# Optimization experiments

Hardware: AMD Instinct MI355X
Metric: run time of the kernel (lower is better)

The kernel has to match this reference:

```python
import jax, jax.numpy as jnp
import numpy as np

N_NODES = 50000
N_EDGES = 600000
N_GRAPHS = 256
BN_EPS = 1e-5
NEG_SLOPE = 0.2  # PyG GATv2 default leaky_relu slope


def segment_softmax(logits, seg, num_segments):
    # logits: [E, H], softmax over edges sharing the same destination node
    m = jax.ops.segment_max(logits, seg, num_segments=num_segments)
    e = jnp.exp(logits - m[seg])
    s = jax.ops.segment_sum(e, seg, num_segments=num_segments)
    return e / (s[seg] + 1e-16)


def gatv2_layer(h, edge_attr, src, dst, Wl, bl, Wr, br, We, att, bias, concat):
    # PyG GATv2Conv (share_weights=False, edge_dim set), eval mode (no dropout)
    heads, out_c = att.shape
    N = h.shape[0]
    xl = (h @ Wl + bl).reshape(N, heads, out_c)  # messages from source
    xr = (h @ Wr + br).reshape(N, heads, out_c)  # destination term
    em = (edge_attr @ We).reshape(-1, heads, out_c)
    z = jax.nn.leaky_relu(xl[src] + xr[dst] + em, NEG_SLOPE)  # [E,H,C]
    logits = jnp.einsum('ehc,hc->eh', z, att)
    alpha = segment_softmax(logits, dst, N)  # [E,H]
    out = jax.ops.segment_sum(xl[src] * alpha[:, :, None], dst, num_segments=N)
    out = out.reshape(N, heads * out_c) if concat else out.mean(axis=1)
    return out + bias


def batch_norm(h, gamma, beta):
    mu = h.mean(axis=0)
    var = h.var(axis=0)
    return gamma * (h - mu) * jax.lax.rsqrt(var + BN_EPS) + beta


def setup_inputs() -> dict:
    key = jax.random.key(0)
    ks = jax.random.split(key, 32)
    F, Fe, H, C = 64, 16, 4, 64
    HC = H * C

    def w(k, shape):
        return jax.random.normal(k, shape, dtype=jnp.float32) * 0.1

    inp = {
        'x': jax.random.normal(ks[0], (N_NODES, F), dtype=jnp.float32),
        'edge_attr': jax.random.normal(ks[1], (N_EDGES, Fe), dtype=jnp.float32),
        'edge_index': jax.random.randint(ks[2], (2, N_EDGES), 0, N_NODES, dtype=jnp.int32),
        'batch': jnp.sort(jax.random.randint(ks[3], (N_NODES,), 0, N_GRAPHS, dtype=jnp.int32)),
        # input projection
        'W_in': w(ks[4], (F, C)), 'b_in': jnp.zeros((C,), jnp.float32),
        'Wl0': w(ks[5], (C, HC)), 'bl0': jnp.zeros((HC,), jnp.float32),
        'Wr0': w(ks[6], (C, HC)), 'br0': jnp.zeros((HC,), jnp.float32),
        'We0': w(ks[7], (Fe, HC)),
        'att0': w(ks[8], (H, C)), 'bias0': jnp.zeros((HC,), jnp.float32),
        'g0': jnp.ones((HC,), jnp.float32), 'beta0': jnp.zeros((HC,), jnp.float32),
        'Wl1': w(ks[9], (HC, HC)), 'bl1': jnp.zeros((HC,), jnp.float32),
        'Wr1': w(ks[10], (HC, HC)), 'br1': jnp.zeros((HC,), jnp.float32),
        'We1': w(ks[11], (Fe, HC)),
        'att1': w(ks[12], (H, C)), 'bias1': jnp.zeros((C,), jnp.float32),
        'g1': jnp.ones((C,), jnp.float32), 'beta1': jnp.zeros((C,), jnp.float32),
        # MLP head 64 -> 32 -> 16 -> 1
        'Wm1': w(ks[13], (C, C // 2)), 'bm1': jnp.zeros((C // 2,), jnp.float32),
        'Wm2': w(ks[14], (C // 2, C // 4)), 'bm2': jnp.zeros((C // 4,), jnp.float32),
        'Wm3': w(ks[15], (C // 4, 1)), 'bm3': jnp.zeros((1,), jnp.float32),
    }
    return inp


def reference(x, edge_attr, W_in, b_in,
              Wl0, bl0, Wr0, br0, We0, att0, bias0, g0, beta0,
              Wl1, bl1, Wr1, br1, We1, att1, bias1, g1, beta1,
              Wm1, bm1, Wm2, bm2, Wm3, bm3,
              edge_index, batch):
    src, dst = edge_index[0], edge_index[1]
    h = jax.nn.relu(x @ W_in + b_in)
    h = gatv2_layer(h, edge_attr, src, dst, Wl0, bl0, Wr0, br0, We0, att0, bias0, True)
    h = batch_norm(h, g0, beta0)
    h = jax.nn.relu(h)  # dropout is identity in eval mode
    h = gatv2_layer(h, edge_attr, src, dst, Wl1, bl1, Wr1, br1, We1, att1, bias1, False)
    h = batch_norm(h, g1, beta1)
    # global mean pool over graphs
    cnt = jax.ops.segment_sum(jnp.ones((h.shape[0],), h.dtype), batch, num_segments=N_GRAPHS)
    pooled = jax.ops.segment_sum(h, batch, num_segments=N_GRAPHS) / jnp.maximum(cnt, 1.0)[:, None]
    z = jax.nn.relu(pooled @ Wm1 + bm1)
    z = jax.nn.relu(z @ Wm2 + bm2)
    return z @ Wm3 + bm3  # [N_GRAPHS, 1]
```

## Files before the change

### kernel.cpp

```cpp
#include <hip/hip_runtime.h>
#include <math.h>

constexpr int NN = 50000;
constexpr int NE = 600000;
constexpr int NG = 256;
constexpr int SB = (NN + 255) / 256;
constexpr float kBnEps = 1e-5f;
constexpr float kSlope = 0.2f;

typedef _Float16 f16x8 __attribute__((ext_vector_type(8)));
typedef float f32x16 __attribute__((ext_vector_type(16)));

__device__ __forceinline__ float rdlane(float v, int l) {
    return __builtin_bit_cast(float, __builtin_amdgcn_readlane(__builtin_bit_cast(int, v), l));
}

template <int CTRL>
__device__ __forceinline__ float dppadd(float v) {
    int t = __builtin_amdgcn_mov_dpp(__builtin_bit_cast(int, v), CTRL, 0xF, 0xF, true);
    return v + __builtin_bit_cast(float, t);
}
__device__ __forceinline__ float sum16(float v) {
    v = dppadd<0xB1>(v);
    v = dppadd<0x4E>(v);
    v = dppadd<0x141>(v);
    v = dppadd<0x140>(v);
    return v;
}

__device__ __forceinline__ float4 fma4(float a, float4 b, float4 c) {
    c.x = fmaf(a, b.x, c.x); c.y = fmaf(a, b.y, c.y);
    c.z = fmaf(a, b.z, c.z); c.w = fmaf(a, b.w, c.w);
    return c;
}

__global__ __launch_bounds__(256) void k_hist(const int* __restrict__ dst, int* __restrict__ cnt)
{
    int e = blockIdx.x * 256 + threadIdx.x;
    if (e < NE) atomicAdd(&cnt[dst[e]], 1);
}

__global__ __launch_bounds__(256) void k_scanA(const int* __restrict__ cnt,
                                               int* __restrict__ offs, int* __restrict__ bsum)
{
    __shared__ int s[256];
    int tid = threadIdx.x;
    int i = blockIdx.x * 256 + tid;
    int v = (i < NN) ? cnt[i] : 0;
    s[tid] = v;
    __syncthreads();
    #pragma unroll
    for (int d = 1; d < 256; d <<= 1) {
        int u = (tid >= d) ? s[tid - d] : 0;
        __syncthreads();
        s[tid] += u;
        __syncthreads();
    }
    if (i < NN) offs[i] = s[tid];
    if (tid == 255) bsum[blockIdx.x] = s[255];
}

__global__ __launch_bounds__(256) void k_scanC(const int* __restrict__ cnt,
                                               const int* __restrict__ bsum,
                                               int* __restrict__ offs, int* __restrict__ cur)
{
    __shared__ int sred[256];
    int t = threadIdx.x;
    int b = blockIdx.x;
    int v = (t < SB && t < b) ? bsum[t] : 0;
    sred[t] = v;
    __syncthreads();
    #pragma unroll
    for (int d = 128; d > 0; d >>= 1) {
        if (t < d) sred[t] += sred[t + d];
        __syncthreads();
    }
    int pre = sred[0];
    int i = b * 256 + t;
    if (i > NN) return;
    if (i == NN) { offs[NN] = NE; return; }
    int w = offs[i] - cnt[i] + pre;
    offs[i] = w;
    cur[i] = w;
}

__global__ __launch_bounds__(256) void k_scatter_light(const int* __restrict__ dst,
                                                       const int* __restrict__ src,
                                                       int* __restrict__ cur,
                                                       int2* __restrict__ se)
{
    int e = blockIdx.x * 256 + threadIdx.x;
    if (e < NE) {
        int p = atomicAdd(&cur[dst[e]], 1);
        se[p] = make_int2(src[e], e);
    }
}

__device__ __forceinline__ void prep_w_body(int T, const float* __restrict__ WL,
                                            const float* __restrict__ WR,
                                            _Float16* __restrict__ bhi,
                                            _Float16* __restrict__ blo)
{
    int g   = T & 1;
    int col = (T >> 1) & 511;
    int kt  = T >> 10;
    const float* W = (col < 256) ? WL : WR;
    int c = col & 255;
    f16x8 h8, l8;
    #pragma unroll
    for (int i = 0; i < 8; ++i) {
        float v = W[(size_t)(kt * 16 + g * 8 + i) * 256 + c];
        _Float16 hv = (_Float16)v;
        h8[i] = hv;
        l8[i] = (_Float16)(v - (float)hv);
    }
    *(f16x8*)(bhi + (size_t)T * 8) = h8;
    *(f16x8*)(blo + (size_t)T * 8) = l8;
}

__global__ __launch_bounds__(256) void k_prep_all(
    const float* __restrict__ Wl0, const float* __restrict__ Wr0,
    _Float16* __restrict__ bhi0, _Float16* __restrict__ blo0,
    const float* __restrict__ Wl1, const float* __restrict__ Wr1,
    _Float16* __restrict__ bhi1, _Float16* __restrict__ blo1)
{
    if (blockIdx.x < 16) {
        int T = blockIdx.x * 256 + threadIdx.x;
        prep_w_body(T, Wl0, Wr0, bhi0, blo0);
    } else {
        int T = (blockIdx.x - 16) * 256 + threadIdx.x;
        prep_w_body(T, Wl1, Wr1, bhi1, blo1);
    }
}

__global__ __launch_bounds__(512) void k_lin0_mfma(
    const float* __restrict__ x, const float* __restrict__ Win,
    const float* __restrict__ bin,
    const _Float16* __restrict__ Bhi, const _Float16* __restrict__ Blo,
    const float* __restrict__ bl, const float* __restrict__ br,
    float* __restrict__ outl, float* __restrict__ outr)
{
    __shared__ float h0s[64][68];
    __shared__ f16x8 Apack[2][4][128];
    int tid = threadIdx.x;
    int lane = tid & 63, wave = tid >> 6;
    int row0 = blockIdx.x * 64;

    {
        int rbase = row0 + wave * 8;
        float xreg[8];
        #pragma unroll
        for (int j = 0; j < 8; ++j) {
            int row = rbase + j; if (row >= NN) row = NN - 1;
            xreg[j] = x[(size_t)row * 64 + lane];
        }
        float b0 = bin[lane];
        float h0r[8];
        #pragma unroll
        for (int j = 0; j < 8; ++j) h0r[j] = b0;
        for (int k = 0; k < 64; ++k) {
            float w = Win[k * 64 + lane];
            #pragma unroll
            for (int j = 0; j < 8; ++j) h0r[j] = fmaf(rdlane(xreg[j], k), w, h0r[j]);
        }
        #pragma unroll
        for (int j = 0; j < 8; ++j)
            h0s[wave * 8 + j][lane] = fmaxf(h0r[j], 0.f);
    }
    __syncthreads();

    {
        int row = tid >> 3;
        int o = (tid & 7) * 8;
        f16x8 hi8, lo8;
        #pragma unroll
        for (int i = 0; i < 8; ++i) {
            float v = h0s[row][o + i];
            _Float16 hv = (_Float16)v;
            hi8[i] = hv;
            lo8[i] = (_Float16)(v - (float)hv);
        }
        int kt = o >> 4, g2 = (o >> 3) & 1;
        int slot = (g2 * 64 + row) ^ kt;
        Apack[0][kt][slot] = hi8;
        Apack[1][kt][slot] = lo8;
    }
    __syncthreads();

    int g = lane >> 5;
    int rowtile = wave >> 2;
    int colbase = (wave & 3) * 128 + (lane & 31);
    int aslot = g * 64 + rowtile * 32 + (lane & 31);
    f32x16 acc[4];
    #pragma unroll
    for (int nt = 0; nt < 4; ++nt)
        #pragma unroll
        for (int r = 0; r < 16; ++r) acc[nt][r] = 0.f;

    const f16x8* bh = (const f16x8*)Bhi;
    const f16x8* bo = (const f16x8*)Blo;
    size_t fbase = (size_t)colbase * 2 + g;

    #pragma unroll 1
    for (int kt = 0; kt < 4; ++kt) {
        f16x8 ahi = Apack[0][kt][aslot ^ kt];
        f16x8 alo = Apack[1][kt][aslot ^ kt];
        f16x8 wh[4], wl[4];
        #pragma unroll
        for (int nt = 0; nt < 4; ++nt) {
            size_t fi = fbase + (size_t)kt * 1024 + nt * 64;
            wh[nt] = bh[fi];
            wl[nt] = bo[fi];
        }
        #pragma unroll
        for (int nt = 0; nt < 4; ++nt)
            acc[nt] = __builtin_amdgcn_mfma_f32_32x32x16_f16(ahi, wh[nt], acc[nt], 0, 0, 0);
        #pragma unroll
        for (int nt = 0; nt < 4; ++nt)
            acc[nt] = __builtin_amdgcn_mfma_f32_32x32x16_f16(alo, wh[nt], acc[nt], 0, 0, 0);
        #pragma unroll
        for (int nt = 0; nt < 4; ++nt)
            acc[nt] = __builtin_amdgcn_mfma_f32_32x32x16_f16(ahi, wl[nt], acc[nt], 0, 0, 0);
    }

    #pragma unroll
    for (int nt = 0; nt < 4; ++nt) {
        int col = colbase + nt * 32;
        bool isR = col >= 256;
        int c = isR ? col - 256 : col;
        float bv = isR ? br[c] : bl[c];
        float* outp = isR ? outr : outl;
        #pragma unroll
        for (int r = 0; r < 16; ++r) {
            int rowoff = (r & 3) + 8 * (r >> 2) + 4 * g;
            int grow = row0 + rowtile * 32 + rowoff;
            if (grow < NN)
                outp[(size_t)grow * 256 + c] = acc[nt][r] + bv;
        }
    }
}

__global__ __launch_bounds__(256) void k_linear2_mfma(
    const float* __restrict__ h, const _Float16* __restrict__ Bhi,
    const _Float16* __restrict__ Blo, const float* __restrict__ bl,
    const float* __restrict__ br, const float* __restrict__ scale,
    const float* __restrict__ shift, float* __restrict__ outl,
    float* __restrict__ outr)
{
    __shared__ f16x8 Apack[2][16][64];
    int tid = threadIdx.x;
    int lane = tid & 63, wave = tid >> 6;
    int q = blockIdx.x & 3;
    int mslot = blockIdx.x >> 2;
    int g = lane >> 5;
    int colbase = q * 128 + wave * 32 + (lane & 31);
    size_t fbase = (size_t)colbase * 2 + g;

    const f16x8* bh = (const f16x8*)Bhi;
    const f16x8* bo = (const f16x8*)Blo;
    f16x8 BH[16], BL[16];
    #pragma unroll
    for (int kt = 0; kt < 16; ++kt) {
        BH[kt] = bh[fbase + (size_t)kt * 1024];
        BL[kt] = bo[fbase + (size_t)kt * 1024];
    }

    bool isR = colbase >= 256;
    int c = isR ? colbase - 256 : colbase;
    float bv = isR ? br[c] : bl[c];
    float* outp = isR ? outr : outl;

    constexpr int NT = (NN + 31) / 32;
    for (int t = mslot; t < NT; t += 128) {
        int row0 = t * 32;
        {
            int row  = tid >> 3;
            int koff = (tid & 7) * 32;
            int grow = row0 + row; if (grow >= NN) grow = NN - 1;
            const float* hp = h + (size_t)grow * 256 + koff;
            #pragma unroll
            for (int j2 = 0; j2 < 4; ++j2) {
                int o = koff + j2 * 8;
                float4 a  = *(const float4*)(hp + j2 * 8);
                float4 b  = *(const float4*)(hp + j2 * 8 + 4);
                float4 s0 = *(const float4*)(scale + o);
                float4 s1 = *(const float4*)(scale + o + 4);
                float4 f0 = *(const float4*)(shift + o);
                float4 f1 = *(const float4*)(shift + o + 4);
                float va[8] = {
                    fmaxf(fmaf(a.x, s0.x, f0.x), 0.f), fmaxf(fmaf(a.y, s0.y, f0.y), 0.f),
                    fmaxf(fmaf(a.z, s0.z, f0.z), 0.f), fmaxf(fmaf(a.w, s0.w, f0.w), 0.f),
                    fmaxf(fmaf(b.x, s1.x, f1.x), 0.f), fmaxf(fmaf(b.y, s1.y, f1.y), 0.f),
                    fmaxf(fmaf(b.z, s1.z, f1.z), 0.f), fmaxf(fmaf(b.w, s1.w, f1.w), 0.f)};
                f16x8 hi8, lo8;
                #pragma unroll
                for (int i = 0; i < 8; ++i) {
                    _Float16 hv = (_Float16)va[i];
                    hi8[i] = hv;
                    lo8[i] = (_Float16)(va[i] - (float)hv);
                }
                int kt = o >> 4, g2 = (o >> 3) & 1;
                int slot = (g2 * 32 + row) ^ (kt & 7);
                Apack[0][kt][slot] = hi8;
                Apack[1][kt][slot] = lo8;
            }
        }
        __syncthreads();

        f32x16 acc;
        #pragma unroll
        for (int r = 0; r < 16; ++r) acc[r] = 0.f;

        #pragma unroll
        for (int kt = 0; kt < 16; ++kt) {
            f16x8 ahi = Apack[0][kt][lane ^ (kt & 7)];
            f16x8 alo = Apack[1][kt][lane ^ (kt & 7)];
            acc = __builtin_amdgcn_mfma_f32_32x32x16_f16(ahi, BH[kt], acc, 0, 0, 0);
            acc = __builtin_amdgcn_mfma_f32_32x32x16_f16(alo, BH[kt], acc, 0, 0, 0);
            acc = __builtin_amdgcn_mfma_f32_32x32x16_f16(ahi, BL[kt], acc, 0, 0, 0);
        }
        __syncthreads();

        #pragma unroll
        for (int r = 0; r < 16; ++r) {
            int rowoff = (r & 3) + 8 * (r >> 2) + 4 * g;
            int grow = row0 + rowoff;
            if (grow < NN)
                outp[(size_t)grow * 256 + c] = acc[r] + bv;
        }
    }
}

template <bool CONCAT, int NPW>
__global__ __launch_bounds__(256) void k_attn(
    const float* __restrict__ xl, const float* __restrict__ xr,
    const int2* __restrict__ se, const float* __restrict__ ea,
    const float* __restrict__ We, const float* __restrict__ att,
    const int* __restrict__ offs, const float* __restrict__ bias,
    float* __restrict__ out)
{
    int tid = threadIdx.x;
    int lane = tid & 63, wave = tid >> 6;
    float4 wr[16];
    #pragma unroll
    for (int k = 0; k < 16; ++k) wr[k] = ((const float4*)(We + k * 256))[lane];
    float4 ar = ((const float4*)att)[lane];

    int g16 = lane >> 4;
    int k16 = lane & 15;
    int nodebase = (blockIdx.x * 4 + wave) * NPW;
    if (nodebase >= NN) return;

    for (int nn = 0; nn < NPW; ++nn) {
        int n = nodebase + nn;
        if (n >= NN) break;
        int beg = offs[n], end = offs[n + 1];
        float4 xr4 = ((const float4*)(xr + (size_t)n * 256))[lane];

        float m = -INFINITY, ssum = 0.f;
        float4 acc = make_float4(0.f, 0.f, 0.f, 0.f);

        float nea = 0.f;
        float4 nx0, nx1, nx2, nx3;

        auto loadbatch = [&](int i) {
            int idx = i + g16;
            if (idx > end - 1) idx = end - 1;
            int2 sv2 = se[idx];
            nea = ea[(size_t)sv2.y * 16 + k16];
            int sv = sv2.x;
            int s0 = __builtin_amdgcn_readlane(sv, 0);
            int s1 = __builtin_amdgcn_readlane(sv, 16);
            int s2 = __builtin_amdgcn_readlane(sv, 32);
            int s3 = __builtin_amdgcn_readlane(sv, 48);
            nx0 = ((const float4*)(xl + (size_t)s0 * 256))[lane];
            nx1 = ((const float4*)(xl + (size_t)s1 * 256))[lane];
            nx2 = ((const float4*)(xl + (size_t)s2 * 256))[lane];
            nx3 = ((const float4*)(xl + (size_t)s3 * 256))[lane];
        };

        if (beg < end) loadbatch(beg);

        for (int i = beg; i < end; i += 4) {
            float cea = nea;
            float4 x0 = nx0, x1 = nx1, x2 = nx2, x3 = nx3;
            if (i + 4 < end) loadbatch(i + 4);

            float p[4];
            #pragma unroll
            for (int g = 0; g < 4; ++g) {
                float4 xg = (g == 0) ? x0 : (g == 1) ? x1 : (g == 2) ? x2 : x3;
                float4 em = xr4;
                #pragma unroll
                for (int k = 0; k < 16; ++k) {
                    float a = rdlane(cea, g * 16 + k);
                    em.x = fmaf(a, wr[k].x, em.x);
                    em.y = fmaf(a, wr[k].y, em.y);
                    em.z = fmaf(a, wr[k].z, em.z);
                    em.w = fmaf(a, wr[k].w, em.w);
                }
                float z0 = xg.x + em.x;
                float z1 = xg.y + em.y;
                float z2 = xg.z + em.z;
                float z3 = xg.w + em.w;
                z0 = (z0 > 0.f) ? z0 : kSlope * z0;
                z1 = (z1 > 0.f) ? z1 : kSlope * z1;
                z2 = (z2 > 0.f) ? z2 : kSlope * z2;
                z3 = (z3 > 0.f) ? z3 : kSlope * z3;
                float pv = fmaf(z0, ar.x, fmaf(z1, ar.y, fmaf(z2, ar.z, z3 * ar.w)));
                pv = sum16(pv);
                p[g] = (i + g < end) ? pv : -INFINITY;
            }
            float pm = fmaxf(fmaxf(p[0], p[1]), fmaxf(p[2], p[3]));
            float mn = fmaxf(m, pm);
            float sc = __expf(m - mn);
            float w0 = __expf(p[0] - mn);
            float w1 = __expf(p[1] - mn);
            float w2 = __expf(p[2] - mn);
            float w3 = __expf(p[3] - mn);
            ssum = fmaf(ssum, sc, (w0 + w1) + (w2 + w3));
            acc.x = fmaf(acc.x, sc, fmaf(w0, x0.x, fmaf(w1, x1.x, fmaf(w2, x2.x, w3 * x3.x))));
            acc.y = fmaf(acc.y, sc, fmaf(w0, x0.y, fmaf(w1, x1.y, fmaf(w2, x2.y, w3 * x3.y))));
            acc.z = fmaf(acc.z, sc, fmaf(w0, x0.z, fmaf(w1, x1.z, fmaf(w2, x2.z, w3 * x3.z))));
            acc.w = fmaf(acc.w, sc, fmaf(w0, x0.w, fmaf(w1, x1.w, fmaf(w2, x2.w, w3 * x3.w))));
            m = mn;
        }

        float inv = 1.f / (ssum + 1e-16f);
        if (CONCAT) {
            float4 b4 = ((const float4*)bias)[lane];
            float4 o;
            o.x = fmaf(acc.x, inv, b4.x);
            o.y = fmaf(acc.y, inv, b4.y);
            o.z = fmaf(acc.z, inv, b4.z);
            o.w = fmaf(acc.w, inv, b4.w);
            ((float4*)(out + (size_t)n * 256))[lane] = o;
        } else {
            float v0 = acc.x * inv, v1 = acc.y * inv, v2 = acc.z * inv, v3 = acc.w * inv;
            v0 += __shfl_xor(v0, 16, 64); v0 += __shfl_xor(v0, 32, 64);
            v1 += __shfl_xor(v1, 16, 64); v1 += __shfl_xor(v1, 32, 64);
            v2 += __shfl_xor(v2, 16, 64); v2 += __shfl_xor(v2, 32, 64);
            v3 += __shfl_xor(v3, 16, 64); v3 += __shfl_xor(v3, 32, 64);
            if (lane < 16) {
                float4 b4 = ((const float4*)bias)[lane];
                float4 o;
                o.x = fmaf(0.25f, v0, b4.x);
                o.y = fmaf(0.25f, v1, b4.y);
                o.z = fmaf(0.25f, v2, b4.z);
                o.w = fmaf(0.25f, v3, b4.w);
                ((float4*)(out + (size_t)n * 64))[lane] = o;
            }
        }
    }
}

template <int CH>
__global__ __launch_bounds__(256) void k_bn_stats(const float* __restrict__ h,
                                                  float* __restrict__ sum,
                                                  float* __restrict__ sumsq)
{
    constexpr int RP = 256 / CH;
    int tid = threadIdx.x;
    int c = tid % CH;
    int rsub = tid / CH;
    float s = 0.f, q = 0.f;
    #pragma unroll 4
    for (int n = blockIdx.x * RP + rsub; n < NN; n += gridDim.x * RP) {
        float v = h[(size_t)n * CH + c];
        s += v; q = fmaf(v, v, q);
    }
    __shared__ float ls[256], lq[256];
    ls[tid] = s; lq[tid] = q;
    __syncthreads();
    if (tid < CH) {
        #pragma unroll
        for (int r = 1; r < RP; ++r) { s += ls[tid + r * CH]; q += lq[tid + r * CH]; }
        atomicAdd(&sum[tid], s);
        atomicAdd(&sumsq[tid], q);
    }
}

__global__ void k_bn_finalize(const float* __restrict__ sum, const float* __restrict__ sumsq,
                              const float* __restrict__ g, const float* __restrict__ beta,
                              float* __restrict__ scale, float* __restrict__ shift, int CH)
{
    int c = threadIdx.x;
    if (c >= CH) return;
    float inv_n = 1.f / (float)NN;
    float mu = sum[c] * inv_n;
    float var = sumsq[c] * inv_n - mu * mu;
    float sc = g[c] / sqrtf(var + kBnEps);
    scale[c] = sc;
    shift[c] = fmaf(-mu, sc, beta[c]);
}

__global__ __launch_bounds__(256) void k_pool_mlp(
    const float* __restrict__ h2, const float* __restrict__ bns,
    const float* __restrict__ bnq, const float* __restrict__ gam,
    const float* __restrict__ beta, const int* __restrict__ batch,
    const float* __restrict__ Wm1, const float* __restrict__ bm1,
    const float* __restrict__ Wm2, const float* __restrict__ bm2,
    const float* __restrict__ Wm3, const float* __restrict__ bm3,
    float* __restrict__ out)
{
    int g = blockIdx.x, tid = threadIdx.x;
    int lane = tid & 63, wave = tid >> 6;
    __shared__ int sb[2];
    if (tid < 2) {
        int target = g + tid;
        int lo = 0, hi = NN;
        while (lo < hi) {
            int mid = (lo + hi) >> 1;
            if (batch[mid] < target) lo = mid + 1; else hi = mid;
        }
        sb[tid] = lo;
    }
    __syncthreads();
    int s = sb[0], e = sb[1];
    float inv_n = 1.f / (float)NN;
    float mu = bns[lane] * inv_n;
    float var = bnq[lane] * inv_n - mu * mu;
    float sc = gam[lane] / sqrtf(var + kBnEps);
    float sh = fmaf(-mu, sc, beta[lane]);
    float acc = 0.f;
    #pragma unroll 4
    for (int n = s + wave; n < e; n += 4)
        acc += fmaf(h2[(size_t)n * 64 + lane], sc, sh);
    __shared__ float red[4][64];
    red[wave][lane] = acc;
    __syncthreads();
    __shared__ float p[64], z1[32], z2[16];
    if (tid < 64) {
        float cnt = (float)(e - s);
        float a = red[0][tid] + red[1][tid] + red[2][tid] + red[3][tid];
        p[tid] = a / fmaxf(cnt, 1.f);
    }
    __syncthreads();
    if (tid < 32) {
        float a = bm1[tid];
        #pragma unroll
        for (int k = 0; k < 64; ++k) a = fmaf(p[k], Wm1[k * 32 + tid], a);
        z1[tid] = fmaxf(a, 0.f);
    }
    __syncthreads();
    if (tid < 16) {
        float a = bm2[tid];
        #pragma unroll
        for (int k = 0; k < 32; ++k) a = fmaf(z1[k], Wm2[k * 16 + tid], a);
        z2[tid] = fmaxf(a, 0.f);
    }
    __syncthreads();
    if (tid == 0) {
        float a = bm3[0];
        #pragma unroll
        for (int k = 0; k < 16; ++k) a = fmaf(z2[k], Wm3[k], a);
        out[g] = a;
    }
}

extern "C" void kernel_launch(void* const* d_in, const int* in_sizes, int n_in,
                              void* d_out, int out_size, void* d_ws, size_t ws_size,
                              hipStream_t stream)
{
    const float* x     = (const float*)d_in[0];
    const float* ea    = (const float*)d_in[1];
    const int*   ei    = (const int*)d_in[2];
    const int*   bat   = (const int*)d_in[3];
    const float* W_in  = (const float*)d_in[4];
    const float* b_in  = (const float*)d_in[5];
    const float* Wl0   = (const float*)d_in[6];
    const float* bl0   = (const float*)d_in[7];
    const float* Wr0   = (const float*)d_in[8];
    const float* br0   = (const float*)d_in[9];
    const float* We0   = (const float*)d_in[10];
    const float* att0  = (const float*)d_in[11];
    const float* bias0 = (const float*)d_in[12];
    const float* g0    = (const float*)d_in[13];
    const float* beta0 = (const float*)d_in[14];
    const float* Wl1   = (const float*)d_in[15];
    const float* bl1   = (const float*)d_in[16];
    const float* Wr1   = (const float*)d_in[17];
    const float* br1   = (const float*)d_in[18];
    const float* We1   = (const float*)d_in[19];
    const float* att1  = (const float*)d_in[20];
    const float* bias1 = (const float*)d_in[21];
    const float* g1    = (const float*)d_in[22];
    const float* beta1 = (const float*)d_in[23];
    const float* Wm1   = (const float*)d_in[24];
    const float* bm1   = (const float*)d_in[25];
    const float* Wm2   = (const float*)d_in[26];
    const float* bm2   = (const float*)d_in[27];
    const float* Wm3   = (const float*)d_in[28];
    const float* bm3   = (const float*)d_in[29];
    const int* src = ei;
    const int* dst = ei + NE;
    float* out = (float*)d_out;

    char* p = (char*)d_ws;
    auto take = [&](size_t nbytes) -> char* {
        char* q = p;
        p += (nbytes + 255) & ~(size_t)255;
        return q;
    };
    char* z0 = p;
    int*   hist   = (int*)take((size_t)NN * 4);
    float* bns0   = (float*)take(256 * 4);
    float* bnq0   = (float*)take(256 * 4);
    float* bns1   = (float*)take(64 * 4);
    float* bnq1   = (float*)take(64 * 4);
    size_t zbytes = (size_t)(p - z0);
    int*   offs   = (int*)take((size_t)(NN + 1) * 4);
    int*   curs   = (int*)take((size_t)NN * 4);
    int*   bsum   = (int*)take((size_t)SB * 4);
    int2*  se     = (int2*)take((size_t)NE * 8);
    float* h2     = (float*)take((size_t)NN * 64 * 4);
    float* xl     = (float*)take((size_t)NN * 256 * 4);
    float* xr     = (float*)take((size_t)NN * 256 * 4);
    float* h1     = (float*)take((size_t)NN * 256 * 4);
    float* scale0 = (float*)take(256 * 4);
    float* shift0 = (float*)take(256 * 4);
    _Float16* Bhi1 = (_Float16*)take((size_t)256 * 512 * 2);
    _Float16* Blo1 = (_Float16*)take((size_t)256 * 512 * 2);
    _Float16* Bhi0 = (_Float16*)take((size_t)64 * 512 * 2);
    _Float16* Blo0 = (_Float16*)take((size_t)64 * 512 * 2);

    hipMemsetAsync(z0, 0, zbytes, stream);

    k_hist<<<(NE + 255) / 256, 256, 0, stream>>>(dst, hist);
    k_prep_all<<<80, 256, 0, stream>>>(Wl0, Wr0, Bhi0, Blo0, Wl1, Wr1, Bhi1, Blo1);
    k_scanA<<<SB, 256, 0, stream>>>(hist, offs, bsum);
    k_scanC<<<SB, 256, 0, stream>>>(hist, bsum, offs, curs);
    k_scatter_light<<<(NE + 255) / 256, 256, 0, stream>>>(dst, src, curs, se);

    constexpr int NPW = 2;
    int attn_blocks = (NN + 4 * NPW - 1) / (4 * NPW);
    int lin0_blocks = (NN + 63) / 64;

    k_lin0_mfma<<<lin0_blocks, 512, 0, stream>>>(
        x, W_in, b_in, Bhi0, Blo0, bl0, br0, xl, xr);
    k_attn<true, NPW><<<attn_blocks, 256, 0, stream>>>(
        xl, xr, se, ea, We0, att0, offs, bias0, h1);
    k_bn_stats<256><<<1024, 256, 0, stream>>>(h1, bns0, bnq0);
    k_bn_finalize<<<1, 256, 0, stream>>>(bns0, bnq0, g0, beta0, scale0, shift0, 256);

    k_linear2_mfma<<<512, 256, 0, stream>>>(
        h1, Bhi1, Blo1, bl1, br1, scale0, shift0, xl, xr);
    k_attn<false, NPW><<<attn_blocks, 256, 0, stream>>>(
        xl, xr, se, ea, We1, att1, offs, bias1, h2);
    k_bn_stats<64><<<1024, 256, 0, stream>>>(h2, bns1, bnq1);

    k_pool_mlp<<<NG, 256, 0, stream>>>(h2, bns1, bnq1, g1, beta1, bat,
                                       Wm1, bm1, Wm2, bm2, Wm3, bm3, out);
}
```

Measured before the change: 677.0 us.

## Double-buffer A tiles in linear2 and fold BN finalize into the kernel

The second-layer projection kernel now prefetches the next row tile of h1 into registers while running the MFMA loop on the current tile, using a double-buffered LDS A-pack. Only one barrier per iteration remains. The batch-norm finalize step is computed per block into shared memory from the raw sums, which removes a separate single-block kernel launch. In exchange the kernel uses more LDS and registers, which can lower occupancy, and each block redundantly recomputes the 256 BN scale/shift values.

```diff
diff --git a/kernel.cpp b/kernel.cpp
--- a/kernel.cpp
+++ b/kernel.cpp
@@ -243,11 +243,13 @@
 __global__ __launch_bounds__(256) void k_linear2_mfma(
     const float* __restrict__ h, const _Float16* __restrict__ Bhi,
     const _Float16* __restrict__ Blo, const float* __restrict__ bl,
-    const float* __restrict__ br, const float* __restrict__ scale,
-    const float* __restrict__ shift, float* __restrict__ outl,
+    const float* __restrict__ br, const float* __restrict__ bns,
+    const float* __restrict__ bnq, const float* __restrict__ gam,
+    const float* __restrict__ beta, float* __restrict__ outl,
     float* __restrict__ outr)
 {
-    __shared__ f16x8 Apack[2][16][64];
+    __shared__ f16x8 Apack[2][2][16][64];
+    __shared__ float s_scale[256], s_shift[256];
     int tid = threadIdx.x;
     int lane = tid & 63, wave = tid >> 6;
     int q = blockIdx.x & 3;
@@ -256,6 +258,15 @@
     int colbase = q * 128 + wave * 32 + (lane & 31);
     size_t fbase = (size_t)colbase * 2 + g;
 
+    {
+        float inv_n = 1.f / (float)NN;
+        float mu = bns[tid] * inv_n;
+        float var = bnq[tid] * inv_n - mu * mu;
+        float sc = gam[tid] / sqrtf(var + kBnEps);
+        s_scale[tid] = sc;
+        s_shift[tid] = fmaf(-mu, sc, beta[tid]);
+    }
+
     const f16x8* bh = (const f16x8*)Bhi;
     const f16x8* bo = (const f16x8*)Blo;
     f16x8 BH[16], BL[16];
@@ -270,57 +281,74 @@
     float bv = isR ? br[c] : bl[c];
     float* outp = isR ? outr : outl;
 
+    int srow  = tid >> 3;
+    int koff = (tid & 7) * 32;
+
+    auto load_tile = [&](int t, float4* va) {
+        int grow = t * 32 + srow; if (grow >= NN) grow = NN - 1;
+        const float* hp = h + (size_t)grow * 256 + koff;
+        #pragma unroll
+        for (int j = 0; j < 8; ++j) va[j] = *(const float4*)(hp + j * 4);
+    };
+    auto split_store = [&](int buf, const float4* va4) {
+        #pragma unroll
+        for (int j2 = 0; j2 < 4; ++j2) {
+            int o = koff + j2 * 8;
+            float4 a  = va4[j2 * 2];
+            float4 b  = va4[j2 * 2 + 1];
+            float4 s0 = *(const float4*)(s_scale + o);
+            float4 s1 = *(const float4*)(s_scale + o + 4);
+            float4 f0 = *(const float4*)(s_shift + o);
+            float4 f1 = *(const float4*)(s_shift + o + 4);
+            float va[8] = {
+                fmaxf(fmaf(a.x, s0.x, f0.x), 0.f), fmaxf(fmaf(a.y, s0.y, f0.y), 0.f),
+                fmaxf(fmaf(a.z, s0.z, f0.z), 0.f), fmaxf(fmaf(a.w, s0.w, f0.w), 0.f),
+                fmaxf(fmaf(b.x, s1.x, f1.x), 0.f), fmaxf(fmaf(b.y, s1.y, f1.y), 0.f),
+                fmaxf(fmaf(b.z, s1.z, f1.z), 0.f), fmaxf(fmaf(b.w, s1.w, f1.w), 0.f)};
+            f16x8 hi8, lo8;
+            #pragma unroll
+            for (int i = 0; i < 8; ++i) {
+                _Float16 hv = (_Float16)va[i];
+                hi8[i] = hv;
+                lo8[i] = (_Float16)(va[i] - (float)hv);
+            }
+            int kt = o >> 4, g2 = (o >> 3) & 1;
+            int slot = (g2 * 32 + srow) ^ (kt & 7);
+            Apack[buf][0][kt][slot] = hi8;
+            Apack[buf][1][kt][slot] = lo8;
+        }
+    };
+
     constexpr int NT = (NN + 31) / 32;
+
+    {
+        float4 va[8];
+        load_tile(mslot, va);
+        __syncthreads();
+        split_store(0, va);
+    }
+    __syncthreads();
+
+    int cur = 0;
     for (int t = mslot; t < NT; t += 128) {
-        int row0 = t * 32;
-        {
-            int row  = tid >> 3;
-            int koff = (tid & 7) * 32;
-            int grow = row0 + row; if (grow >= NN) grow = NN - 1;
-            const float* hp = h + (size_t)grow * 256 + koff;
-            #pragma unroll
-            for (int j2 = 0; j2 < 4; ++j2) {
-                int o = koff + j2 * 8;
-                float4 a  = *(const float4*)(hp + j2 * 8);
-                float4 b  = *(const float4*)(hp + j2 * 8 + 4);
-                float4 s0 = *(const float4*)(scale + o);
-                float4 s1 = *(const float4*)(scale + o + 4);
-                float4 f0 = *(const float4*)(shift + o);
-                float4 f1 = *(const float4*)(shift + o + 4);
-                float va[8] = {
-                    fmaxf(fmaf(a.x, s0.x, f0.x), 0.f), fmaxf(fmaf(a.y, s0.y, f0.y), 0.f),
-                    fmaxf(fmaf(a.z, s0.z, f0.z), 0.f), fmaxf(fmaf(a.w, s0.w, f0.w), 0.f),
-                    fmaxf(fmaf(b.x, s1.x, f1.x), 0.f), fmaxf(fmaf(b.y, s1.y, f1.y), 0.f),
-                    fmaxf(fmaf(b.z, s1.z, f1.z), 0.f), fmaxf(fmaf(b.w, s1.w, f1.w), 0.f)};
-                f16x8 hi8, lo8;
-                #pragma unroll
-                for (int i = 0; i < 8; ++i) {
-                    _Float16 hv = (_Float16)va[i];
-                    hi8[i] = hv;
-                    lo8[i] = (_Float16)(va[i] - (float)hv);
-                }
-                int kt = o >> 4, g2 = (o >> 3) & 1;
-                int slot = (g2 * 32 + row) ^ (kt & 7);
-                Apack[0][kt][slot] = hi8;
-                Apack[1][kt][slot] = lo8;
-            }
-        }
-        __syncthreads();
+        int tn = t + 128;
+        bool more = tn < NT;
+        float4 vb[8];
+        if (more) load_tile(tn, vb);
 
         f32x16 acc;
         #pragma unroll
         for (int r = 0; r < 16; ++r) acc[r] = 0.f;
-
         #pragma unroll
         for (int kt = 0; kt < 16; ++kt) {
-            f16x8 ahi = Apack[0][kt][lane ^ (kt & 7)];
-            f16x8 alo = Apack[1][kt][lane ^ (kt & 7)];
+            f16x8 ahi = Apack[cur][0][kt][lane ^ (kt & 7)];
+            f16x8 alo = Apack[cur][1][kt][lane ^ (kt & 7)];
             acc = __builtin_amdgcn_mfma_f32_32x32x16_f16(ahi, BH[kt], acc, 0, 0, 0);
             acc = __builtin_amdgcn_mfma_f32_32x32x16_f16(alo, BH[kt], acc, 0, 0, 0);
             acc = __builtin_amdgcn_mfma_f32_32x32x16_f16(ahi, BL[kt], acc, 0, 0, 0);
         }
-        __syncthreads();
-
+
+        int row0 = t * 32;
         #pragma unroll
         for (int r = 0; r < 16; ++r) {
             int rowoff = (r & 3) + 8 * (r >> 2) + 4 * g;
@@ -328,6 +356,10 @@
             if (grow < NN)
                 outp[(size_t)grow * 256 + c] = acc[r] + bv;
         }
+
+        if (more) split_store(cur ^ 1, vb);
+        __syncthreads();
+        cur ^= 1;
     }
 }
 
@@ -480,20 +512,6 @@
     }
 }
 
-__global__ void k_bn_finalize(const float* __restrict__ sum, const float* __restrict__ sumsq,
-                              const float* __restrict__ g, const float* __restrict__ beta,
-                              float* __restrict__ scale, float* __restrict__ shift, int CH)
-{
-    int c = threadIdx.x;
-    if (c >= CH) return;
-    float inv_n = 1.f / (float)NN;
-    float mu = sum[c] * inv_n;
-    float var = sumsq[c] * inv_n - mu * mu;
-    float sc = g[c] / sqrtf(var + kBnEps);
-    scale[c] = sc;
-    shift[c] = fmaf(-mu, sc, beta[c]);
-}
-
 __global__ __launch_bounds__(256) void k_pool_mlp(
     const float* __restrict__ h2, const float* __restrict__ bns,
     const float* __restrict__ bnq, const float* __restrict__ gam,
@@ -617,8 +635,6 @@
     float* xl     = (float*)take((size_t)NN * 256 * 4);
     float* xr     = (float*)take((size_t)NN * 256 * 4);
     float* h1     = (float*)take((size_t)NN * 256 * 4);
-    float* scale0 = (float*)take(256 * 4);
-    float* shift0 = (float*)take(256 * 4);
     _Float16* Bhi1 = (_Float16*)take((size_t)256 * 512 * 2);
     _Float16* Blo1 = (_Float16*)take((size_t)256 * 512 * 2);
     _Float16* Bhi0 = (_Float16*)take((size_t)64 * 512 * 2);
@@ -641,10 +657,9 @@
     k_attn<true, NPW><<<attn_blocks, 256, 0, stream>>>(
         xl, xr, se, ea, We0, att0, offs, bias0, h1);
     k_bn_stats<256><<<1024, 256, 0, stream>>>(h1, bns0, bnq0);
-    k_bn_finalize<<<1, 256, 0, stream>>>(bns0, bnq0, g0, beta0, scale0, shift0, 256);
 
     k_linear2_mfma<<<512, 256, 0, stream>>>(
-        h1, Bhi1, Blo1, bl1, br1, scale0, shift0, xl, xr);
+        h1, Bhi1, Blo1, bl1, br1, bns0, bnq0, g0, beta0, xl, xr);
     k_attn<false, NPW><<<attn_blocks, 256, 0, stream>>>(
         xl, xr, se, ea, We1, att1, offs, bias1, h2);
     k_bn_stats<64><<<1024, 256, 0, stream>>>(h2, bns1, bnq1);
```

Result: no change. 689.1 us (+1.8%).
